# Performance work log

Measured on AMD Instinct MI355X. Metric: run time of the kernel, lower is better.

## Reference

```python
import jax, jax.numpy as jnp
import numpy as np

DIM = 2048
N_HEAD = 16
HEAD_DIM = DIM // N_HEAD


def setup_inputs() -> dict:
    key = jax.random.key(0)
    ks = jax.random.split(key, 7)
    B, N = 2, 2048
    s = 1.0 / np.sqrt(DIM)
    return {
        "x": jax.random.normal(ks[0], (B, N, DIM), dtype=jnp.float32),
        "Wq": jax.random.normal(ks[1], (DIM, DIM), dtype=jnp.float32) * s,
        "bq": jnp.zeros((DIM,), dtype=jnp.float32),
        "Wkv": jax.random.normal(ks[2], (DIM, 2 * HEAD_DIM), dtype=jnp.float32) * s,
        "bkv": jnp.zeros((2 * HEAD_DIM,), dtype=jnp.float32),
        "Wo": jax.random.normal(ks[3], (DIM, DIM), dtype=jnp.float32) * s,
        "bo": jnp.zeros((DIM,), dtype=jnp.float32),
    }


def reference(x, Wq, bq, Wkv, bkv, Wo, bo):
    B, N, D = x.shape
    # Q projection -> (B, H, N, hd)
    q = (x @ Wq + bq).reshape(B, N, N_HEAD, HEAD_DIM).transpose(0, 2, 1, 3)
    # shared single-head K/V (kv = x, self-attention path)
    kvp = x @ Wkv + bkv  # (B, M, 2*hd)
    k, v = kvp[..., :HEAD_DIM], kvp[..., HEAD_DIM:]  # (B, M, hd) each
    scale = 1.0 / np.sqrt(HEAD_DIM).astype(np.float32)
    # broadcast shared K over heads without materializing expanded K/V
    scores = jnp.einsum("bhnd,bmd->bhnm", q, k) * scale  # (B, H, N, M)
    attn = jax.nn.softmax(scores, axis=-1)
    out = jnp.einsum("bhnm,bmd->bhnd", attn, v)  # (B, H, N, hd)
    out = out.transpose(0, 2, 1, 3).reshape(B, N, D)
    return out @ Wo + bo
```

## Files before the change

### kernel.cpp

```cpp
#include <hip/hip_runtime.h>
#include <math.h>

using bf16x8 = __attribute__((ext_vector_type(8))) short;
using f32x4  = __attribute__((ext_vector_type(4))) float;
using f32x16 = __attribute__((ext_vector_type(16))) float;
using u16x4  = __attribute__((ext_vector_type(4))) unsigned short;
using u32x4  = __attribute__((ext_vector_type(4))) unsigned int;

#define DIMSZ 2048
#define NSEQ  2048
#define BATCH 2
#define NHEAD 16
#define HD    128

__device__ __forceinline__ unsigned short f2bf(float x) {
    unsigned int u = __builtin_bit_cast(unsigned int, x);
    unsigned int r = (u + 0x7FFFu + ((u >> 16) & 1u)) >> 16;
    return (unsigned short)r;
}

__device__ __forceinline__ unsigned int cvtpk_bf16(float lo, float hi) {
    unsigned int r;
    asm("v_cvt_pk_bf16_f32 %0, %1, %2" : "=v"(r) : "v"(lo), "v"(hi));
    return r;
}

__device__ __forceinline__ void gload_lds16(const unsigned short* g, unsigned short* l) {
    __builtin_amdgcn_global_load_lds(
        (const __attribute__((address_space(1))) unsigned int*)g,
        (__attribute__((address_space(3))) unsigned int*)l, 16, 0, 0);
}

__global__ void k_cast_bf16(const float* __restrict__ in, unsigned short* __restrict__ out, int n4) {
    int i = blockIdx.x * blockDim.x + threadIdx.x;
    if (i >= n4) return;
    f32x4 v = *(const f32x4*)(in + (size_t)i * 4);
    u16x4 o;
#pragma unroll
    for (int j = 0; j < 4; j++) o[j] = f2bf(v[j]);
    *(u16x4*)(out + (size_t)i * 4) = o;
}

__global__ void k_transpose_w(const float* __restrict__ W, unsigned short* __restrict__ WT,
                              int K, int N, float scale) {
    __shared__ float t[32][33];
    int k0 = blockIdx.y * 32, n0 = blockIdx.x * 32;
    int tx = threadIdx.x, ty = threadIdx.y;
#pragma unroll
    for (int i = 0; i < 32; i += 8) t[ty + i][tx] = W[(size_t)(k0 + ty + i) * N + n0 + tx];
    __syncthreads();
#pragma unroll
    for (int i = 0; i < 32; i += 8) WT[(size_t)(n0 + ty + i) * K + k0 + tx] = f2bf(t[tx][ty + i] * scale);
}

__global__ void k_transpose_v(const unsigned short* __restrict__ kvp, unsigned short* __restrict__ vt) {
    __shared__ unsigned short t[32][33];
    int n0 = blockIdx.x * 32, d0 = blockIdx.y * 32, b = blockIdx.z;
    int tx = threadIdx.x, ty = threadIdx.y;
#pragma unroll
    for (int i = 0; i < 32; i += 8)
        t[ty + i][tx] = kvp[(size_t)(b * NSEQ + n0 + ty + i) * 256 + 128 + d0 + tx];
    __syncthreads();
#pragma unroll
    for (int i = 0; i < 32; i += 8)
        vt[(size_t)(b * HD + d0 + ty + i) * NSEQ + n0 + tx] = t[tx][ty + i];
}

__global__ __launch_bounds__(256, 2)
void k_gemm_qkv(const unsigned short* __restrict__ A, const unsigned short* __restrict__ Bt,
                const float* __restrict__ bq, float bscale, const float* __restrict__ bkv,
                unsigned short* __restrict__ qout, unsigned short* __restrict__ kvout,
                int M, int K) {
    __shared__ unsigned short As[2][128 * 32];
    __shared__ unsigned short Bs[2][128 * 32];
    const int tid = threadIdx.x;
    const int wid = tid >> 6;
    const int lane = tid & 63;
    const int g = lane >> 4, cc = lane & 15;
    const int wr = wid >> 1, wc = wid & 1;
    const size_t m0 = (size_t)blockIdx.y * 128;
    const size_t n0 = (size_t)blockIdx.x * 128;

    f32x4 acc[4][4] = {};

    const int srow = wid * 32 + (lane >> 2);
    const int sch = lane & 3;
    const unsigned short* gA = A + (m0 + srow) * (size_t)K + sch * 8;
    const unsigned short* gB = Bt + (n0 + srow) * (size_t)K + sch * 8;
    const int lo = wid * 32 * 32;

    auto STAGE = [&](int buf, int k0) {
        gload_lds16(gA + k0, &As[buf][lo]);
        gload_lds16(gA + 16 * (size_t)K + k0, &As[buf][lo + 16 * 32]);
        gload_lds16(gB + k0, &Bs[buf][lo]);
        gload_lds16(gB + 16 * (size_t)K + k0, &Bs[buf][lo + 16 * 32]);
    };

    STAGE(0, 0);
    __syncthreads();
    int cur = 0;
    for (int k0 = 0; k0 < K; k0 += 32) {
        if (k0 + 32 < K) STAGE(cur ^ 1, k0 + 32);
        bf16x8 af[4], bfr[4];
#pragma unroll
        for (int mi = 0; mi < 4; mi++) af[mi] = *(const bf16x8*)(&As[cur][(wr * 64 + mi * 16 + cc) * 32 + g * 8]);
#pragma unroll
        for (int ni = 0; ni < 4; ni++) bfr[ni] = *(const bf16x8*)(&Bs[cur][(wc * 64 + ni * 16 + cc) * 32 + g * 8]);
#pragma unroll
        for (int mi = 0; mi < 4; mi++)
#pragma unroll
            for (int ni = 0; ni < 4; ni++)
                acc[mi][ni] = __builtin_amdgcn_mfma_f32_16x16x32_bf16(af[mi], bfr[ni], acc[mi][ni], 0, 0, 0);
        __syncthreads();
        cur ^= 1;
    }

    const bool isQ = (n0 < 2048);
    const int colg = (int)n0 + wc * 64 + cc;
    const int col0 = isQ ? colg : colg - 2048;
    const int ostride = isQ ? 2048 : 256;
    unsigned short* outp = isQ ? qout : kvout;
    float bia[4];
#pragma unroll
    for (int ni = 0; ni < 4; ni++)
        bia[ni] = isQ ? bq[col0 + ni * 16] * bscale : bkv[col0 + ni * 16];
#pragma unroll
    for (int mi = 0; mi < 4; mi++) {
        size_t row = m0 + wr * 64 + mi * 16 + g * 4;
#pragma unroll
        for (int ni = 0; ni < 4; ni++)
#pragma unroll
            for (int r = 0; r < 4; r++)
                outp[(row + r) * ostride + col0 + ni * 16] = f2bf(acc[mi][ni][r] + bia[ni]);
    }
}

__global__ __launch_bounds__(256, 2)
void k_gemm_bt_f32(const unsigned short* __restrict__ A, const unsigned short* __restrict__ Bt,
                   const float* __restrict__ bias, float* __restrict__ Cout,
                   int M, int N, int K) {
    __shared__ unsigned short As[2][128 * 32];
    __shared__ unsigned short Bs[2][128 * 32];
    const int tid = threadIdx.x;
    const int wid = tid >> 6;
    const int lane = tid & 63;
    const int g = lane >> 4, cc = lane & 15;
    const int wr = wid >> 1, wc = wid & 1;
    const size_t m0 = (size_t)blockIdx.y * 128;
    const size_t n0 = (size_t)blockIdx.x * 128;

    f32x4 acc[4][4] = {};

    const int srow = wid * 32 + (lane >> 2);
    const int sch = lane & 3;
    const unsigned short* gA = A + (m0 + srow) * (size_t)K + sch * 8;
    const unsigned short* gB = Bt + (n0 + srow) * (size_t)K + sch * 8;
    const int lo = wid * 32 * 32;

    auto STAGE = [&](int buf, int k0) {
        gload_lds16(gA + k0, &As[buf][lo]);
        gload_lds16(gA + 16 * (size_t)K + k0, &As[buf][lo + 16 * 32]);
        gload_lds16(gB + k0, &Bs[buf][lo]);
        gload_lds16(gB + 16 * (size_t)K + k0, &Bs[buf][lo + 16 * 32]);
    };

    STAGE(0, 0);
    __syncthreads();
    int cur = 0;
    for (int k0 = 0; k0 < K; k0 += 32) {
        if (k0 + 32 < K) STAGE(cur ^ 1, k0 + 32);
        bf16x8 af[4], bfr[4];
#pragma unroll
        for (int mi = 0; mi < 4; mi++) af[mi] = *(const bf16x8*)(&As[cur][(wr * 64 + mi * 16 + cc) * 32 + g * 8]);
#pragma unroll
        for (int ni = 0; ni < 4; ni++) bfr[ni] = *(const bf16x8*)(&Bs[cur][(wc * 64 + ni * 16 + cc) * 32 + g * 8]);
#pragma unroll
        for (int mi = 0; mi < 4; mi++)
#pragma unroll
            for (int ni = 0; ni < 4; ni++)
                acc[mi][ni] = __builtin_amdgcn_mfma_f32_16x16x32_bf16(af[mi], bfr[ni], acc[mi][ni], 0, 0, 0);
        __syncthreads();
        cur ^= 1;
    }

    const int col0 = (int)n0 + wc * 64 + cc;
    float bia[4];
#pragma unroll
    for (int ni = 0; ni < 4; ni++) bia[ni] = bias[col0 + ni * 16];
#pragma unroll
    for (int mi = 0; mi < 4; mi++) {
        size_t row = m0 + wr * 64 + mi * 16 + g * 4;
#pragma unroll
        for (int ni = 0; ni < 4; ni++)
#pragma unroll
            for (int r = 0; r < 4; r++)
                Cout[(row + r) * N + col0 + ni * 16] = acc[mi][ni][r] + bia[ni];
    }
}

__global__ __launch_bounds__(256, 2)
void k_attn(const unsigned short* __restrict__ q, const unsigned short* __restrict__ kvp,
            const unsigned short* __restrict__ vt, unsigned short* __restrict__ out) {
    __shared__ unsigned char Kb[2][16384];
    __shared__ unsigned char Vb[2][16384];

    const int b = blockIdx.z, h = blockIdx.y, qt = blockIdx.x;
    const int tid = threadIdx.x, w = tid >> 6, lane = tid & 63;
    const int q32 = lane & 31, hi = lane >> 5;

    const int qrow = qt * 128 + w * 32 + q32;
    const unsigned short* qp = q + (size_t)(b * NSEQ + qrow) * DIMSZ + h * HD + hi * 8;
    bf16x8 qf[8];
#pragma unroll
    for (int dc = 0; dc < 8; dc++) qf[dc] = *(const bf16x8*)(qp + dc * 16);

    const char* kvpc = (const char*)kvp;
    const char* vtc  = (const char*)vt;
    size_t srcK[4], srcV[4];
#pragma unroll
    for (int c = 0; c < 4; c++) {
        unsigned int o = (tid + c * 256) * 16;
        unsigned int krow = o >> 8, kcol = o & 255;
        srcK[c] = (size_t)(b * NSEQ + krow) * 512 + (kcol ^ (((krow >> 1) & 15) << 4));
        unsigned int vrow = o >> 7, vcol = o & 127;
        srcV[c] = (size_t)(b * HD + vrow) * 4096 + (vcol ^ (((vrow >> 2) & 7) << 4));
    }

    auto STAGE = [&](int buf, int t) {
        size_t kb_ = (size_t)t * 32768;
        size_t vb_ = (size_t)t * 128;
#pragma unroll
        for (int c = 0; c < 4; c++) {
            gload_lds16((const unsigned short*)(kvpc + srcK[c] + kb_),
                        (unsigned short*)(Kb[buf] + (w * 64 + c * 256) * 16));
            gload_lds16((const unsigned short*)(vtc + srcV[c] + vb_),
                        (unsigned short*)(Vb[buf] + (w * 64 + c * 256) * 16));
        }
    };

    f32x16 o0 = {}, o1 = {}, o2 = {}, o3 = {};
    float l_run = 0.0f;
    const unsigned int swK = ((q32 >> 1) & 15) << 4;
    const unsigned int swV = ((q32 >> 2) & 7) << 4;

#define PROC_KT(S, KTB)                                                               \
    {                                                                                 \
        float pz[16];                                                                 \
        _Pragma("unroll") for (int r = 0; r < 16; r++) {                              \
            pz[r] = exp2f(S[r]);                                                      \
            l_run += pz[r];                                                           \
        }                                                                             \
        _Pragma("unroll") for (int kc = 0; kc < 2; kc++) {                            \
            unsigned int own01 = cvtpk_bf16(pz[kc * 8 + 0], pz[kc * 8 + 1]);          \
            unsigned int own23 = cvtpk_bf16(pz[kc * 8 + 2], pz[kc * 8 + 3]);          \
            unsigned int own45 = cvtpk_bf16(pz[kc * 8 + 4], pz[kc * 8 + 5]);          \
            unsigned int own67 = cvtpk_bf16(pz[kc * 8 + 6], pz[kc * 8 + 7]);          \
            unsigned int send_a = hi ? own01 : own45;                                 \
            unsigned int send_b = hi ? own23 : own67;                                 \
            unsigned int got_a = (unsigned int)__shfl_xor((int)send_a, 32, 64);       \
            unsigned int got_b = (unsigned int)__shfl_xor((int)send_b, 32, 64);       \
            u32x4 awv;                                                                \
            awv[0] = hi ? got_a : own01;                                              \
            awv[1] = hi ? got_b : own23;                                              \
            awv[2] = hi ? own45 : got_a;                                              \
            awv[3] = hi ? own67 : got_b;                                              \
            bf16x8 pa = __builtin_bit_cast(bf16x8, awv);                              \
            const unsigned int kbo = (KTB) + kc * 32 + hi * 16;                       \
            bf16x8 vf0 = *(const bf16x8*)(Vc + (q32 + 0) * 128 + (kbo ^ swV));        \
            bf16x8 vf1 = *(const bf16x8*)(Vc + (q32 + 32) * 128 + (kbo ^ swV));       \
            bf16x8 vf2 = *(const bf16x8*)(Vc + (q32 + 64) * 128 + (kbo ^ swV));       \
            bf16x8 vf3 = *(const bf16x8*)(Vc + (q32 + 96) * 128 + (kbo ^ swV));       \
            __builtin_amdgcn_s_setprio(1);                                            \
            o0 = __builtin_amdgcn_mfma_f32_32x32x16_bf16(pa, vf0, o0, 0, 0, 0);       \
            o1 = __builtin_amdgcn_mfma_f32_32x32x16_bf16(pa, vf1, o1, 0, 0, 0);       \
            o2 = __builtin_amdgcn_mfma_f32_32x32x16_bf16(pa, vf2, o2, 0, 0, 0);       \
            o3 = __builtin_amdgcn_mfma_f32_32x32x16_bf16(pa, vf3, o3, 0, 0, 0);       \
            __builtin_amdgcn_s_setprio(0);                                            \
        }                                                                             \
    }

    STAGE(0, 0);
    __syncthreads();

    for (int t = 0; t < NSEQ / 64; t++) {
        const int cur = t & 1;
        if (t < NSEQ / 64 - 1) STAGE(cur ^ 1, t + 1);

        const unsigned char* Kc = Kb[cur];
        const unsigned char* Vc = Vb[cur];

        f32x16 s0 = {}, s1 = {};
#pragma unroll
        for (int dc = 0; dc < 8; dc++) {
            const unsigned int db = dc * 32 + hi * 16;
            bf16x8 kf0 = *(const bf16x8*)(Kc + q32 * 256 + (db ^ swK));
            bf16x8 kf1 = *(const bf16x8*)(Kc + (q32 + 32) * 256 + (db ^ swK));
            __builtin_amdgcn_s_setprio(1);
            s0 = __builtin_amdgcn_mfma_f32_32x32x16_bf16(kf0, qf[dc], s0, 0, 0, 0);
            s1 = __builtin_amdgcn_mfma_f32_32x32x16_bf16(kf1, qf[dc], s1, 0, 0, 0);
            __builtin_amdgcn_s_setprio(0);
        }

        PROC_KT(s0, 0)
        PROC_KT(s1, 64)

        __syncthreads();
    }
#undef PROC_KT

    l_run += __shfl_xor(l_run, 32, 64);
    float* Lp = (float*)(Kb[0] + w * 128);
    if (hi == 0) Lp[q32] = l_run;

    float rinv[16];
#pragma unroll
    for (int r = 0; r < 16; r++) {
        int qloc = (r & 3) + 8 * (r >> 2) + 4 * hi;
        rinv[r] = 1.0f / Lp[qloc];
    }

    unsigned short* op = out + (size_t)(b * NSEQ + qt * 128 + w * 32) * DIMSZ + h * HD + q32;
#pragma unroll
    for (int r = 0; r < 16; r++) {
        int qloc = (r & 3) + 8 * (r >> 2) + 4 * hi;
        op[(size_t)qloc * DIMSZ + 0]  = f2bf(o0[r] * rinv[r]);
        op[(size_t)qloc * DIMSZ + 32] = f2bf(o1[r] * rinv[r]);
        op[(size_t)qloc * DIMSZ + 64] = f2bf(o2[r] * rinv[r]);
        op[(size_t)qloc * DIMSZ + 96] = f2bf(o3[r] * rinv[r]);
    }
}

extern "C" void kernel_launch(void* const* d_in, const int* in_sizes, int n_in,
                              void* d_out, int out_size, void* d_ws, size_t ws_size,
                              hipStream_t stream) {
    const float* x   = (const float*)d_in[0];
    const float* Wq  = (const float*)d_in[1];
    const float* bq  = (const float*)d_in[2];
    const float* Wkv = (const float*)d_in[3];
    const float* bkv = (const float*)d_in[4];
    const float* Wo  = (const float*)d_in[5];
    const float* bo  = (const float*)d_in[6];

    char* w = (char*)d_ws;
    unsigned short* xb    = (unsigned short*)(w);
    unsigned short* wqkvt = (unsigned short*)(w + 16777216);
    unsigned short* wot   = (unsigned short*)(w + 26214400);
    unsigned short* qb    = (unsigned short*)(w + 34603008);
    unsigned short* kvpb  = (unsigned short*)(w + 51380224);
    unsigned short* vtb   = (unsigned short*)(w + 53477376);
    unsigned short* aob   = xb;

    const float sc = 0.08838834764831845f * 1.4426950408889634f;

    k_cast_bf16<<<dim3((BATCH * NSEQ * DIMSZ / 4 + 255) / 256), dim3(256), 0, stream>>>(
        x, xb, BATCH * NSEQ * DIMSZ / 4);
    k_transpose_w<<<dim3(DIMSZ / 32, DIMSZ / 32), dim3(32, 8), 0, stream>>>(Wq, wqkvt, DIMSZ, DIMSZ, sc);
    k_transpose_w<<<dim3(256 / 32, DIMSZ / 32), dim3(32, 8), 0, stream>>>(
        Wkv, wqkvt + (size_t)2048 * 2048, DIMSZ, 256, 1.0f);
    k_transpose_w<<<dim3(DIMSZ / 32, DIMSZ / 32), dim3(32, 8), 0, stream>>>(Wo, wot, DIMSZ, DIMSZ, 1.0f);

    k_gemm_qkv<<<dim3(2304 / 128, BATCH * NSEQ / 128), dim3(256), 0, stream>>>(
        xb, wqkvt, bq, sc, bkv, qb, kvpb, BATCH * NSEQ, DIMSZ);
    k_transpose_v<<<dim3(NSEQ / 32, HD / 32, BATCH), dim3(32, 8), 0, stream>>>(kvpb, vtb);
    k_attn<<<dim3(NSEQ / 128, NHEAD, BATCH), dim3(256), 0, stream>>>(qb, kvpb, vtb, aob);
    k_gemm_bt_f32<<<dim3(DIMSZ / 128, BATCH * NSEQ / 128), dim3(256), 0, stream>>>(
        aob, wot, bo, (float*)d_out, BATCH * NSEQ, DIMSZ, DIMSZ);
}
```

Before: 218.6 us.

## Process two query tiles per attention block to reuse staged K/V

Each attention workgroup now handles 256 query rows, as two 128-row sets A and B per wave, instead of 128. Every K and V fragment read from LDS feeds twice as many MFMAs, and global K/V staging traffic per query is halved. The grid is halved, launch bounds drop to one block per CU to allow double the accumulator registers, and the setprio hints are removed. The risk is fewer resident waves (256 blocks on the GPU) and heavy register pressure or spills.

```diff
diff --git a/kernel.cpp b/kernel.cpp
--- a/kernel.cpp
+++ b/kernel.cpp
@@ -198,7 +198,7 @@
     }
 }
 
-__global__ __launch_bounds__(256, 2)
+__global__ __launch_bounds__(256, 1)
 void k_attn(const unsigned short* __restrict__ q, const unsigned short* __restrict__ kvp,
             const unsigned short* __restrict__ vt, unsigned short* __restrict__ out) {
     __shared__ unsigned char Kb[2][16384];
@@ -208,11 +208,15 @@
     const int tid = threadIdx.x, w = tid >> 6, lane = tid & 63;
     const int q32 = lane & 31, hi = lane >> 5;
 
-    const int qrow = qt * 128 + w * 32 + q32;
-    const unsigned short* qp = q + (size_t)(b * NSEQ + qrow) * DIMSZ + h * HD + hi * 8;
-    bf16x8 qf[8];
-#pragma unroll
-    for (int dc = 0; dc < 8; dc++) qf[dc] = *(const bf16x8*)(qp + dc * 16);
+    const int qrowA = qt * 256 + w * 32 + q32;
+    const unsigned short* qpA = q + (size_t)(b * NSEQ + qrowA) * DIMSZ + h * HD + hi * 8;
+    const unsigned short* qpB = qpA + (size_t)128 * DIMSZ;
+    bf16x8 qfA[8], qfB[8];
+#pragma unroll
+    for (int dc = 0; dc < 8; dc++) {
+        qfA[dc] = *(const bf16x8*)(qpA + dc * 16);
+        qfB[dc] = *(const bf16x8*)(qpB + dc * 16);
+    }
 
     const char* kvpc = (const char*)kvp;
     const char* vtc  = (const char*)vt;
@@ -238,44 +242,50 @@
         }
     };
 
-    f32x16 o0 = {}, o1 = {}, o2 = {}, o3 = {};
-    float l_run = 0.0f;
+    f32x16 oA[4] = {}, oB[4] = {};
+    float l_runA = 0.0f, l_runB = 0.0f;
     const unsigned int swK = ((q32 >> 1) & 15) << 4;
     const unsigned int swV = ((q32 >> 2) & 7) << 4;
 
-#define PROC_KT(S, KTB)                                                               \
+#define PROC2(SA, SB, KTB)                                                            \
     {                                                                                 \
-        float pz[16];                                                                 \
+        float pzA[16], pzB[16];                                                       \
         _Pragma("unroll") for (int r = 0; r < 16; r++) {                              \
-            pz[r] = exp2f(S[r]);                                                      \
-            l_run += pz[r];                                                           \
+            pzA[r] = exp2f(SA[r]);                                                    \
+            l_runA += pzA[r];                                                         \
+            pzB[r] = exp2f(SB[r]);                                                    \
+            l_runB += pzB[r];                                                         \
         }                                                                             \
         _Pragma("unroll") for (int kc = 0; kc < 2; kc++) {                            \
-            unsigned int own01 = cvtpk_bf16(pz[kc * 8 + 0], pz[kc * 8 + 1]);          \
-            unsigned int own23 = cvtpk_bf16(pz[kc * 8 + 2], pz[kc * 8 + 3]);          \
-            unsigned int own45 = cvtpk_bf16(pz[kc * 8 + 4], pz[kc * 8 + 5]);          \
-            unsigned int own67 = cvtpk_bf16(pz[kc * 8 + 6], pz[kc * 8 + 7]);          \
-            unsigned int send_a = hi ? own01 : own45;                                 \
-            unsigned int send_b = hi ? own23 : own67;                                 \
-            unsigned int got_a = (unsigned int)__shfl_xor((int)send_a, 32, 64);       \
-            unsigned int got_b = (unsigned int)__shfl_xor((int)send_b, 32, 64);       \
-            u32x4 awv;                                                                \
-            awv[0] = hi ? got_a : own01;                                              \
-            awv[1] = hi ? got_b : own23;                                              \
-            awv[2] = hi ? own45 : got_a;                                              \
-            awv[3] = hi ? own67 : got_b;                                              \
-            bf16x8 pa = __builtin_bit_cast(bf16x8, awv);                              \
+            unsigned int a01 = cvtpk_bf16(pzA[kc * 8 + 0], pzA[kc * 8 + 1]);          \
+            unsigned int a23 = cvtpk_bf16(pzA[kc * 8 + 2], pzA[kc * 8 + 3]);          \
+            unsigned int a45 = cvtpk_bf16(pzA[kc * 8 + 4], pzA[kc * 8 + 5]);          \
+            unsigned int a67 = cvtpk_bf16(pzA[kc * 8 + 6], pzA[kc * 8 + 7]);          \
+            unsigned int b01 = cvtpk_bf16(pzB[kc * 8 + 0], pzB[kc * 8 + 1]);          \
+            unsigned int b23 = cvtpk_bf16(pzB[kc * 8 + 2], pzB[kc * 8 + 3]);          \
+            unsigned int b45 = cvtpk_bf16(pzB[kc * 8 + 4], pzB[kc * 8 + 5]);          \
+            unsigned int b67 = cvtpk_bf16(pzB[kc * 8 + 6], pzB[kc * 8 + 7]);          \
+            unsigned int gAa = (unsigned int)__shfl_xor((int)(hi ? a01 : a45), 32, 64); \
+            unsigned int gAb = (unsigned int)__shfl_xor((int)(hi ? a23 : a67), 32, 64); \
+            unsigned int gBa = (unsigned int)__shfl_xor((int)(hi ? b01 : b45), 32, 64); \
+            unsigned int gBb = (unsigned int)__shfl_xor((int)(hi ? b23 : b67), 32, 64); \
+            u32x4 wvA, wvB;                                                           \
+            wvA[0] = hi ? gAa : a01;                                                  \
+            wvA[1] = hi ? gAb : a23;                                                  \
+            wvA[2] = hi ? a45 : gAa;                                                  \
+            wvA[3] = hi ? a67 : gAb;                                                  \
+            wvB[0] = hi ? gBa : b01;                                                  \
+            wvB[1] = hi ? gBb : b23;                                                  \
+            wvB[2] = hi ? b45 : gBa;                                                  \
+            wvB[3] = hi ? b67 : gBb;                                                  \
+            bf16x8 paA = __builtin_bit_cast(bf16x8, wvA);                             \
+            bf16x8 paB = __builtin_bit_cast(bf16x8, wvB);                             \
             const unsigned int kbo = (KTB) + kc * 32 + hi * 16;                       \
-            bf16x8 vf0 = *(const bf16x8*)(Vc + (q32 + 0) * 128 + (kbo ^ swV));        \
-            bf16x8 vf1 = *(const bf16x8*)(Vc + (q32 + 32) * 128 + (kbo ^ swV));       \
-            bf16x8 vf2 = *(const bf16x8*)(Vc + (q32 + 64) * 128 + (kbo ^ swV));       \
-            bf16x8 vf3 = *(const bf16x8*)(Vc + (q32 + 96) * 128 + (kbo ^ swV));       \
-            __builtin_amdgcn_s_setprio(1);                                            \
-            o0 = __builtin_amdgcn_mfma_f32_32x32x16_bf16(pa, vf0, o0, 0, 0, 0);       \
-            o1 = __builtin_amdgcn_mfma_f32_32x32x16_bf16(pa, vf1, o1, 0, 0, 0);       \
-            o2 = __builtin_amdgcn_mfma_f32_32x32x16_bf16(pa, vf2, o2, 0, 0, 0);       \
-            o3 = __builtin_amdgcn_mfma_f32_32x32x16_bf16(pa, vf3, o3, 0, 0, 0);       \
-            __builtin_amdgcn_s_setprio(0);                                            \
+            _Pragma("unroll") for (int dt = 0; dt < 4; dt++) {                        \
+                bf16x8 vf = *(const bf16x8*)(Vc + (q32 + 32 * dt) * 128 + (kbo ^ swV)); \
+                oA[dt] = __builtin_amdgcn_mfma_f32_32x32x16_bf16(paA, vf, oA[dt], 0, 0, 0); \
+                oB[dt] = __builtin_amdgcn_mfma_f32_32x32x16_bf16(paB, vf, oB[dt], 0, 0, 0); \
+            }                                                                         \
         }                                                                             \
     }
 
@@ -289,44 +299,42 @@
         const unsigned char* Kc = Kb[cur];
         const unsigned char* Vc = Vb[cur];
 
-        f32x16 s0 = {}, s1 = {};
+        f32x16 sA0 = {}, sA1 = {}, sB0 = {}, sB1 = {};
 #pragma unroll
         for (int dc = 0; dc < 8; dc++) {
             const unsigned int db = dc * 32 + hi * 16;
             bf16x8 kf0 = *(const bf16x8*)(Kc + q32 * 256 + (db ^ swK));
             bf16x8 kf1 = *(const bf16x8*)(Kc + (q32 + 32) * 256 + (db ^ swK));
-            __builtin_amdgcn_s_setprio(1);
-            s0 = __builtin_amdgcn_mfma_f32_32x32x16_bf16(kf0, qf[dc], s0, 0, 0, 0);
-            s1 = __builtin_amdgcn_mfma_f32_32x32x16_bf16(kf1, qf[dc], s1, 0, 0, 0);
-            __builtin_amdgcn_s_setprio(0);
+            sA0 = __builtin_amdgcn_mfma_f32_32x32x16_bf16(kf0, qfA[dc], sA0, 0, 0, 0);
+            sA1 = __builtin_amdgcn_mfma_f32_32x32x16_bf16(kf1, qfA[dc], sA1, 0, 0, 0);
+            sB0 = __builtin_amdgcn_mfma_f32_32x32x16_bf16(kf0, qfB[dc], sB0, 0, 0, 0);
+            sB1 = __builtin_amdgcn_mfma_f32_32x32x16_bf16(kf1, qfB[dc], sB1, 0, 0, 0);
         }
 
-        PROC_KT(s0, 0)
-        PROC_KT(s1, 64)
+        PROC2(sA0, sB0, 0)
+        PROC2(sA1, sB1, 64)
 
         __syncthreads();
     }
-#undef PROC_KT
-
-    l_run += __shfl_xor(l_run, 32, 64);
-    float* Lp = (float*)(Kb[0] + w * 128);
-    if (hi == 0) Lp[q32] = l_run;
-
-    float rinv[16];
+#undef PROC2
+
+    l_runA += __shfl_xor(l_runA, 32, 64);
+    l_runB += __shfl_xor(l_runB, 32, 64);
+    float* Lp = (float*)(Kb[0] + w * 256);
+    if (hi == 0) { Lp[q32] = l_runA; Lp[32 + q32] = l_runB; }
+
+    unsigned short* opA = out + (size_t)(b * NSEQ + qt * 256 + w * 32) * DIMSZ + h * HD + q32;
+    unsigned short* opB = opA + (size_t)128 * DIMSZ;
 #pragma unroll
     for (int r = 0; r < 16; r++) {
         int qloc = (r & 3) + 8 * (r >> 2) + 4 * hi;
-        rinv[r] = 1.0f / Lp[qloc];
-    }
-
-    unsigned short* op = out + (size_t)(b * NSEQ + qt * 128 + w * 32) * DIMSZ + h * HD + q32;
-#pragma unroll
-    for (int r = 0; r < 16; r++) {
-        int qloc = (r & 3) + 8 * (r >> 2) + 4 * hi;
-        op[(size_t)qloc * DIMSZ + 0]  = f2bf(o0[r] * rinv[r]);
-        op[(size_t)qloc * DIMSZ + 32] = f2bf(o1[r] * rinv[r]);
-        op[(size_t)qloc * DIMSZ + 64] = f2bf(o2[r] * rinv[r]);
-        op[(size_t)qloc * DIMSZ + 96] = f2bf(o3[r] * rinv[r]);
+        float rA = 1.0f / Lp[qloc];
+        float rB = 1.0f / Lp[32 + qloc];
+#pragma unroll
+        for (int dt = 0; dt < 4; dt++) {
+            opA[(size_t)qloc * DIMSZ + dt * 32] = f2bf(oA[dt][r] * rA);
+            opB[(size_t)qloc * DIMSZ + dt * 32] = f2bf(oB[dt][r] * rB);
+        }
     }
 }
 
@@ -362,7 +370,7 @@
     k_gemm_qkv<<<dim3(2304 / 128, BATCH * NSEQ / 128), dim3(256), 0, stream>>>(
         xb, wqkvt, bq, sc, bkv, qb, kvpb, BATCH * NSEQ, DIMSZ);
     k_transpose_v<<<dim3(NSEQ / 32, HD / 32, BATCH), dim3(32, 8), 0, stream>>>(kvpb, vtb);
-    k_attn<<<dim3(NSEQ / 128, NHEAD, BATCH), dim3(256), 0, stream>>>(qb, kvpb, vtb, aob);
+    k_attn<<<dim3(NSEQ / 256, NHEAD, BATCH), dim3(256), 0, stream>>>(qb, kvpb, vtb, aob);
     k_gemm_bt_f32<<<dim3(DIMSZ / 128, BATCH * NSEQ / 128), dim3(256), 0, stream>>>(
         aob, wot, bo, (float*)d_out, BATCH * NSEQ, DIMSZ, DIMSZ);
 }
```

Result: slower. 239.4 us (+9.5%).
